# Optimization experiments

Measured on AMD Instinct MI355X. Metric: run time of the kernel, lower is better.

The kernel has to match this reference:

```python
import jax, jax.numpy as jnp
import numpy as np

H, E, K = 1024, 8, 2  # hidden_size, num_experts, top_k
B, S = 2, 4096


def setup_inputs() -> dict:
    key = jax.random.key(0)
    ks = jax.random.split(key, 5)
    s = 1.0 / np.sqrt(H)
    return {
        "x": jax.random.normal(ks[0], (B, S, H), dtype=jnp.float32),
        "ln_scale": jnp.ones((H,), jnp.float32),
        "ln_bias": jnp.zeros((H,), jnp.float32),
        "w1": (jax.random.normal(ks[1], (H, H), jnp.float32) * s),
        "b1": jnp.zeros((H,), jnp.float32),
        "w2": (jax.random.normal(ks[2], (H, E), jnp.float32) * s),
        "b2": jnp.zeros((E,), jnp.float32),
        "We": (jax.random.normal(ks[3], (E, H, H), jnp.float32) * s),
        "be": jnp.zeros((E, H), jnp.float32),
    }


def _layernorm(x, scale, bias, eps=1e-5):
    m = jnp.mean(x, axis=-1, keepdims=True)
    v = jnp.var(x, axis=-1, keepdims=True)
    return (x - m) * jax.lax.rsqrt(v + eps) * scale + bias


def reference(x, ln_scale, ln_bias, w1, b1, w2, b2, We, be):
    b, s, h = x.shape
    # --- router (BaseRouter): LN -> MLP -> softmax -> top-k -> renorm ---
    xn = _layernorm(x, ln_scale, ln_bias)
    hmid = jax.nn.relu(xn @ w1 + b1)
    logits = hmid @ w2 + b2                      # [B,S,E]
    probs = jax.nn.softmax(logits, axis=-1)
    topk_p, topk_i = jax.lax.top_k(probs, K)     # [B,S,K]
    topk_p = topk_p / jnp.sum(topk_p, axis=-1, keepdims=True)
    # sparse combine weights [B,S,E]: renormalized top-k gate, 0 elsewhere
    cw = jnp.sum(topk_p[..., None] * jax.nn.one_hot(topk_i, E, dtype=x.dtype), axis=-2)
    # --- expert dispatch / weighted combine ---
    t = b * s
    xf = x.reshape(t, h)
    cwf = cw.reshape(t, E)
    ye = jnp.einsum('th,ehd->etd', xf, We) + be[:, None, :]   # [E,T,H]
    out = jnp.einsum('te,etd->td', cwf, ye).reshape(b, s, h)
    # --- aux load-balance loss ---
    mean_p = jnp.mean(probs, axis=(0, 1))        # [E]
    aux = jnp.sum(mean_p * jnp.log(mean_p * E + 1e-9))
    return out, aux
```

## Files before the change

### kernel.cpp

```cpp
#include <hip/hip_runtime.h>
#include <hip/hip_fp16.h>

#define H 1024
#define E 8
#define TT 8192

typedef __attribute__((ext_vector_type(8))) short bf16x8;
typedef __attribute__((ext_vector_type(4))) float f32x4;

__device__ __forceinline__ unsigned short f2bf(float f) {
  unsigned int u = __float_as_uint(f);
  u += 0x7fffu + ((u >> 16) & 1u);
  return (unsigned short)(u >> 16);
}

__device__ __forceinline__ int swz(int row, int c) {
  return (row << 5) | (((c ^ (row >> 1)) & 3) << 3);
}

__device__ __forceinline__ void gld16(void* lds, const void* g) {
  __builtin_amdgcn_global_load_lds((const __attribute__((address_space(1))) void*)g,
                                   (__attribute__((address_space(3))) void*)lds, 16, 0, 0);
}

__global__ __launch_bounds__(64) void k_init(int* cnt, double* psum) {
  int t = threadIdx.x;
  if (t < E) { cnt[t] = 0; psum[t] = 0.0; }
}

__global__ __launch_bounds__(256) void k_cast_we(const float* __restrict__ we, unsigned short* __restrict__ wet) {
  __shared__ unsigned short tile[32][33];
  int e = blockIdx.z;
  int kb = blockIdx.x << 5, nb = blockIdx.y << 5;
  int t = threadIdx.x;
  int cc = t & 31, rr = t >> 5;
  size_t base = (size_t)e * H * H;
#pragma unroll
  for (int r = 0; r < 4; ++r) {
    int k = kb + rr + (r << 3);
    tile[rr + (r << 3)][cc] = f2bf(we[base + (size_t)k * H + nb + cc]);
  }
  __syncthreads();
#pragma unroll
  for (int r = 0; r < 4; ++r) {
    int n = nb + rr + (r << 3);
    wet[base + (size_t)n * H + kb + cc] = tile[cc][rr + (r << 3)];
  }
}

__global__ __launch_bounds__(256) void k_cast_w1(const float* __restrict__ w1, const float* __restrict__ lsc,
                                                 unsigned short* __restrict__ w1h, unsigned short* __restrict__ w1l) {
  __shared__ float tile[32][33];
  int kb = blockIdx.x << 5, nb = blockIdx.y << 5;
  int t = threadIdx.x;
  int cc = t & 31, rr = t >> 5;
#pragma unroll
  for (int r = 0; r < 4; ++r) {
    int k = kb + rr + (r << 3);
    tile[rr + (r << 3)][cc] = w1[(size_t)k * H + nb + cc] * lsc[k];
  }
  __syncthreads();
#pragma unroll
  for (int r = 0; r < 4; ++r) {
    int n = nb + rr + (r << 3);
    float v = tile[cc][rr + (r << 3)];
    unsigned short h = f2bf(v);
    float hv = __uint_as_float((unsigned)h << 16);
    unsigned short l = f2bf(v - hv);
    w1h[(size_t)n * H + kb + cc] = h;
    w1l[(size_t)n * H + kb + cc] = l;
  }
}

__global__ __launch_bounds__(256) void k_b1a(const float* __restrict__ w1, const float* __restrict__ lbi,
                                             float* __restrict__ part) {
  int bk = blockIdx.x, t = threadIdx.x;
  float a0 = 0, a1 = 0, a2 = 0, a3 = 0;
  for (int kk = 0; kk < 16; ++kk) {
    int k = (bk << 4) + kk;
    float lb = lbi[k];
    const float* row = &w1[(size_t)k * H];
    a0 = fmaf(lb, row[t], a0);
    a1 = fmaf(lb, row[t + 256], a1);
    a2 = fmaf(lb, row[t + 512], a2);
    a3 = fmaf(lb, row[t + 768], a3);
  }
  part[bk * H + t] = a0;
  part[bk * H + t + 256] = a1;
  part[bk * H + t + 512] = a2;
  part[bk * H + t + 768] = a3;
}

__global__ __launch_bounds__(256) void k_b1b(const float* __restrict__ part, const float* __restrict__ b1,
                                             float* __restrict__ b1eff) {
  int n = (blockIdx.x << 8) + threadIdx.x;
  float s = b1[n];
  for (int j = 0; j < 64; ++j) s += part[j * H + n];
  b1eff[n] = s;
}

__global__ __launch_bounds__(256) void k_stats(const float* __restrict__ x, unsigned short* __restrict__ xb,
                                               unsigned short* __restrict__ zh, unsigned short* __restrict__ zl) {
  int tok = blockIdx.x, t = threadIdx.x;
  const float4 v = *reinterpret_cast<const float4*>(&x[(size_t)tok * H + (t << 2)]);
  float s = v.x + v.y + v.z + v.w;
  float ss = v.x * v.x + v.y * v.y + v.z * v.z + v.w * v.w;
#pragma unroll
  for (int off = 32; off; off >>= 1) { s += __shfl_down(s, off); ss += __shfl_down(ss, off); }
  __shared__ float red[4][2];
  int lane = t & 63, wv = t >> 6;
  if (lane == 0) { red[wv][0] = s; red[wv][1] = ss; }
  __syncthreads();
  float fs = red[0][0] + red[1][0] + red[2][0] + red[3][0];
  float fss = red[0][1] + red[1][1] + red[2][1] + red[3][1];
  float mean = fs * (1.0f / H);
  float var = fss * (1.0f / H) - mean * mean;
  float rstd = rsqrtf(var + 1e-5f);
  float mb = -mean * rstd;
  size_t base = (size_t)tok * H + (t << 2);
  ushort4 ob;
  ob.x = f2bf(v.x); ob.y = f2bf(v.y); ob.z = f2bf(v.z); ob.w = f2bf(v.w);
  *reinterpret_cast<ushort4*>(&xb[base]) = ob;
  float zz[4];
  zz[0] = fmaf(v.x, rstd, mb); zz[1] = fmaf(v.y, rstd, mb);
  zz[2] = fmaf(v.z, rstd, mb); zz[3] = fmaf(v.w, rstd, mb);
  ushort4 oh, ol;
  unsigned u0 = __float_as_uint(zz[0]), u1 = __float_as_uint(zz[1]);
  unsigned u2 = __float_as_uint(zz[2]), u3 = __float_as_uint(zz[3]);
  oh.x = (unsigned short)(u0 >> 16); oh.y = (unsigned short)(u1 >> 16);
  oh.z = (unsigned short)(u2 >> 16); oh.w = (unsigned short)(u3 >> 16);
  float l0 = zz[0] - __uint_as_float(u0 & 0xffff0000u);
  float l1 = zz[1] - __uint_as_float(u1 & 0xffff0000u);
  float l2 = zz[2] - __uint_as_float(u2 & 0xffff0000u);
  float l3 = zz[3] - __uint_as_float(u3 & 0xffff0000u);
  ol.x = (unsigned short)(__float_as_uint(l0) >> 16); ol.y = (unsigned short)(__float_as_uint(l1) >> 16);
  ol.z = (unsigned short)(__float_as_uint(l2) >> 16); ol.w = (unsigned short)(__float_as_uint(l3) >> 16);
  *reinterpret_cast<ushort4*>(&zh[base]) = oh;
  *reinterpret_cast<ushort4*>(&zl[base]) = ol;
}

__global__ __launch_bounds__(256) void k_router_mfma(
    const unsigned short* __restrict__ zh, const unsigned short* __restrict__ zl,
    const unsigned short* __restrict__ w1h,
    const float* __restrict__ b1eff, const float* __restrict__ w2, float* __restrict__ plog) {
  __shared__ __align__(16) short Bt[3][8192];
  int t = threadIdx.x;
  int d = blockIdx.x;
  int l = ((d & 7) << 6) + (d >> 3);
  int bm = (l >> 3) << 7;
  int bnb = l & 7, bn = bnb << 7;
  int w = t >> 6, lane = t & 63;
  int l15 = lane & 15, lgp = lane >> 4;
  int wr = (w >> 1) << 6, wc = (w & 1) << 6;
  int sl = (w << 8) + lane;
  int bo[4];
#pragma unroll
  for (int q = 0; q < 4; ++q) {
    int s = sl + (q << 6);
    int r = s >> 2, cg = (s & 3) ^ ((r >> 1) & 3);
    bo[q] = ((r < 128) ? (bn + r) * H : 1048576 + (bn + r - 128) * H) + (cg << 3);
  }
  int dB = w << 11;
  int zo[4];
#pragma unroll
  for (int i = 0; i < 4; ++i) zo[i] = (bm + wr + (i << 4) + l15) * H + (lgp << 3);
  f32x4 acc[4][4];
#pragma unroll
  for (int i = 0; i < 4; ++i)
#pragma unroll
    for (int j = 0; j < 4; ++j) acc[i][j] = f32x4{0.f, 0.f, 0.f, 0.f};
  bf16x8 ah[3][4], al[3][4];
#pragma unroll
  for (int q = 0; q < 4; ++q) gld16(&Bt[0][dB + (q << 9)], w1h + bo[q]);
#pragma unroll
  for (int q = 0; q < 4; ++q) gld16(&Bt[1][dB + (q << 9)], w1h + bo[q] + 32);
#pragma unroll
  for (int i = 0; i < 4; ++i) {
    ah[0][i] = *(const bf16x8*)(zh + zo[i]);
    al[0][i] = *(const bf16x8*)(zl + zo[i]);
    ah[1][i] = *(const bf16x8*)(zh + zo[i] + 32);
    al[1][i] = *(const bf16x8*)(zl + zo[i] + 32);
  }
#pragma unroll
  for (int kt = 0; kt < 32; ++kt) {
    const int cur = kt % 3;
    if (kt <= 29) {
      const int slot = (kt + 2) % 3, ko = (kt + 2) << 5;
#pragma unroll
      for (int i = 0; i < 4; ++i) {
        ah[slot][i] = *(const bf16x8*)(zh + zo[i] + ko);
        al[slot][i] = *(const bf16x8*)(zl + zo[i] + ko);
      }
    }
    if (kt <= 29) {
      asm volatile("s_waitcnt vmcnt(20)" ::: "memory");
    } else if (kt == 30) {
      asm volatile("s_waitcnt vmcnt(12)" ::: "memory");
    } else {
      asm volatile("s_waitcnt vmcnt(0)" ::: "memory");
    }
    __builtin_amdgcn_sched_barrier(0);
    __builtin_amdgcn_s_barrier();
    __builtin_amdgcn_sched_barrier(0);
    if (kt <= 29) {
      const int bnxt = (kt + 2) % 3, ko = (kt + 2) << 5;
#pragma unroll
      for (int q = 0; q < 4; ++q) gld16(&Bt[bnxt][dB + (q << 9)], w1h + bo[q] + ko);
    }
#pragma unroll
    for (int j = 0; j < 4; ++j) {
      bf16x8 bh = *(const bf16x8*)&Bt[cur][swz(wc + (j << 4) + l15, lgp)];
      bf16x8 bl = *(const bf16x8*)&Bt[cur][swz(128 + wc + (j << 4) + l15, lgp)];
#pragma unroll
      for (int i = 0; i < 4; ++i) {
        acc[i][j] = __builtin_amdgcn_mfma_f32_16x16x32_bf16(ah[cur][i], bh, acc[i][j], 0, 0, 0);
        acc[i][j] = __builtin_amdgcn_mfma_f32_16x16x32_bf16(ah[cur][i], bl, acc[i][j], 0, 0, 0);
        acc[i][j] = __builtin_amdgcn_mfma_f32_16x16x32_bf16(al[cur][i], bh, acc[i][j], 0, 0, 0);
      }
    }
  }
  float w2r[4][8], b1r[4];
#pragma unroll
  for (int j = 0; j < 4; ++j) {
    int col = bn + wc + (j << 4) + l15;
    float4 p0 = *(const float4*)&w2[(size_t)col * E];
    float4 p1 = *(const float4*)&w2[(size_t)col * E + 4];
    w2r[j][0] = p0.x; w2r[j][1] = p0.y; w2r[j][2] = p0.z; w2r[j][3] = p0.w;
    w2r[j][4] = p1.x; w2r[j][5] = p1.y; w2r[j][6] = p1.z; w2r[j][7] = p1.w;
    b1r[j] = b1eff[col];
  }
#pragma unroll
  for (int i = 0; i < 4; ++i)
#pragma unroll
    for (int j = 0; j < 4; ++j)
#pragma unroll
      for (int r = 0; r < 4; ++r) acc[i][j][r] = fmaxf(acc[i][j][r] + b1r[j], 0.f);
  int wh = wc >> 6;
  size_t pbase = ((size_t)(bnb * 2 + wh) * TT + bm) * E;
#pragma unroll
  for (int e = 0; e < E; ++e) {
    float se[4][4];
#pragma unroll
    for (int i = 0; i < 4; ++i)
#pragma unroll
      for (int r = 0; r < 4; ++r)
        se[i][r] = acc[i][0][r] * w2r[0][e] + acc[i][1][r] * w2r[1][e] +
                   acc[i][2][r] * w2r[2][e] + acc[i][3][r] * w2r[3][e];
#pragma unroll
    for (int off = 1; off < 16; off <<= 1)
#pragma unroll
      for (int i = 0; i < 4; ++i)
#pragma unroll
        for (int r = 0; r < 4; ++r) se[i][r] += __shfl_xor(se[i][r], off);
    if (l15 == 0) {
#pragma unroll
      for (int i = 0; i < 4; ++i)
#pragma unroll
        for (int r = 0; r < 4; ++r) {
          int row = wr + (i << 4) + (lgp << 2) + r;
          plog[pbase + (size_t)row * E + e] = se[i][r];
        }
    }
  }
}

__global__ __launch_bounds__(256) void k_top(const float* __restrict__ plog, const float* __restrict__ b2,
                                             int* __restrict__ topE, float* __restrict__ topW,
                                             int* __restrict__ listIdx, float* __restrict__ listW,
                                             int* __restrict__ cnt, double* __restrict__ psum) {
  int t = threadIdx.x, lane = t & 63;
  int tok = (blockIdx.x << 8) + t;
  float lg[E], p[E];
  float4 ba = *reinterpret_cast<const float4*>(b2);
  float4 bb = *reinterpret_cast<const float4*>(b2 + 4);
  lg[0] = ba.x; lg[1] = ba.y; lg[2] = ba.z; lg[3] = ba.w;
  lg[4] = bb.x; lg[5] = bb.y; lg[6] = bb.z; lg[7] = bb.w;
#pragma unroll
  for (int nb = 0; nb < 16; ++nb) {
    const float* pp = &plog[((size_t)nb * TT + tok) * E];
    float4 q0 = *reinterpret_cast<const float4*>(pp);
    float4 q1 = *reinterpret_cast<const float4*>(pp + 4);
    lg[0] += q0.x; lg[1] += q0.y; lg[2] += q0.z; lg[3] += q0.w;
    lg[4] += q1.x; lg[5] += q1.y; lg[6] += q1.z; lg[7] += q1.w;
  }
  float m = lg[0];
#pragma unroll
  for (int e = 1; e < E; ++e) m = fmaxf(m, lg[e]);
  float s = 0.f;
#pragma unroll
  for (int e = 0; e < E; ++e) { p[e] = __expf(lg[e] - m); s += p[e]; }
  float inv = 1.f / s;
#pragma unroll
  for (int e = 0; e < E; ++e) p[e] *= inv;
  {
    float ps[E];
#pragma unroll
    for (int e = 0; e < E; ++e) ps[e] = p[e];
#pragma unroll
    for (int off = 1; off < 64; off <<= 1)
#pragma unroll
      for (int e = 0; e < E; ++e) ps[e] += __shfl_xor(ps[e], off);
    if (lane == 0)
#pragma unroll
      for (int e = 0; e < E; ++e) atomicAdd(&psum[e], (double)ps[e]);
  }
  int e0 = 0;
#pragma unroll
  for (int e = 1; e < E; ++e) if (p[e] > p[e0]) e0 = e;
  int e1 = (e0 == 0) ? 1 : 0;
#pragma unroll
  for (int e = 0; e < E; ++e) if (e != e0 && p[e] > p[e1]) e1 = e;
  float rsw = 1.f / (p[e0] + p[e1]);
  float w0 = p[e0] * rsw, w1v = p[e1] * rsw;
  topE[tok << 1] = e0; topE[(tok << 1) + 1] = e1;
  topW[tok << 1] = w0; topW[(tok << 1) + 1] = w1v;
  unsigned long long lt = (1ull << lane) - 1ull;
#pragma unroll
  for (int e = 0; e < E; ++e) {
    unsigned long long m0 = __ballot(e0 == e);
    unsigned long long m1 = __ballot(e1 == e);
    int n0 = __popcll(m0), total = n0 + __popcll(m1);
    if (total == 0) continue;
    int leader = __ffsll(m0 | m1) - 1;
    int base = 0;
    if (lane == leader) base = atomicAdd(&cnt[e], total);
    base = __shfl(base, leader);
    if (e0 == e) {
      int pos = e * TT + base + __popcll(m0 & lt);
      listIdx[pos] = (tok << 1); listW[pos] = w0;
    }
    if (e1 == e) {
      int pos = e * TT + base + n0 + __popcll(m1 & lt);
      listIdx[pos] = (tok << 1) | 1; listW[pos] = w1v;
    }
  }
}

__global__ __launch_bounds__(256) void k_expert_gemm(const unsigned short* __restrict__ xb,
                                                     const unsigned short* __restrict__ wet,
                                                     const int* __restrict__ listIdx, const float* __restrict__ listW,
                                                     const int* __restrict__ cnt, unsigned short* __restrict__ ys) {
  int d = blockIdx.x;
  int l = ((d & 7) << 8) + (d >> 3);
  int e = l >> 8;
  int lx = l & 255;
  int bx = lx >> 2, by = lx & 3;
  int c = cnt[e];
  int r0 = bx << 7;
  if (r0 >= c) return;
  int n0 = by << 8;
  __shared__ __align__(16) short A[3][4096];
  __shared__ __align__(16) short Bs[3][8192];
  __shared__ int gi[128];
  __shared__ float gw[128];
  int t = threadIdx.x;
  if (t < 128) {
    int rr = r0 + t;
    gi[t] = (rr < c) ? listIdx[e * TT + rr] : -1;
    gw[t] = (rr < c) ? listW[e * TT + rr] : 0.f;
  }
  __syncthreads();
  int w = t >> 6, lane = t & 63;
  int l15 = lane & 15, lgp = lane >> 4;
  int wr = (w >> 1) << 6;
  int wc = (w & 1) << 7;
  int rA0 = t >> 2, cA0 = (t & 3) ^ ((rA0 >> 1) & 3);
  int sA1 = t + 256;
  int rA1 = sA1 >> 2, cA1 = (sA1 & 3) ^ ((rA1 >> 1) & 3);
  int pk0 = gi[rA0], pk1 = gi[rA1];
  const unsigned short* srcA0 = xb + (size_t)((pk0 < 0) ? 0 : (pk0 >> 1)) * H + (cA0 << 3);
  const unsigned short* srcA1 = xb + (size_t)((pk1 < 0) ? 0 : (pk1 >> 1)) * H + (cA1 << 3);
  int ebase = e << 20;
  int boB[4];
#pragma unroll
  for (int q = 0; q < 4; ++q) {
    int s = t + (q << 8);
    int r = s >> 2, cg = (s & 3) ^ ((r >> 1) & 3);
    boB[q] = ebase + (n0 + r) * H + (cg << 3);
  }
  int dA = w << 9;
  int dB = w << 9;
  f32x4 acc[4][8];
#pragma unroll
  for (int i = 0; i < 4; ++i)
#pragma unroll
    for (int j = 0; j < 8; ++j) acc[i][j] = f32x4{0.f, 0.f, 0.f, 0.f};
#pragma unroll
  for (int pt = 0; pt < 3; ++pt) {
    const int ko = pt << 5;
    gld16(&A[pt][dA], srcA0 + ko);
    gld16(&A[pt][dA + 2048], srcA1 + ko);
#pragma unroll
    for (int q = 0; q < 4; ++q) gld16(&Bs[pt][dB + (q << 11)], wet + boB[q] + ko);
  }
#pragma unroll
  for (int kt = 0; kt < 32; ++kt) {
    if (kt <= 29) {
      asm volatile("s_waitcnt vmcnt(12)" ::: "memory");
    } else if (kt == 30) {
      asm volatile("s_waitcnt vmcnt(6)" ::: "memory");
    } else {
      asm volatile("s_waitcnt vmcnt(0)" ::: "memory");
    }
    __builtin_amdgcn_sched_barrier(0);
    __builtin_amdgcn_s_barrier();
    __builtin_amdgcn_sched_barrier(0);
    const int bb = kt % 3;
    bf16x8 aq[4];
#pragma unroll
    for (int i = 0; i < 4; ++i) aq[i] = *(const bf16x8*)&A[bb][swz(wr + (i << 4) + l15, lgp)];
#pragma unroll
    for (int j = 0; j < 8; ++j) {
      bf16x8 bq = *(const bf16x8*)&Bs[bb][swz(wc + (j << 4) + l15, lgp)];
#pragma unroll
      for (int i = 0; i < 4; ++i)
        acc[i][j] = __builtin_amdgcn_mfma_f32_16x16x32_bf16(aq[i], bq, acc[i][j], 0, 0, 0);
    }
    if (kt <= 28) {
      __builtin_amdgcn_sched_barrier(0);
      __builtin_amdgcn_s_barrier();
      const int ko = (kt + 3) << 5;
      gld16(&A[bb][dA], srcA0 + ko);
      gld16(&A[bb][dA + 2048], srcA1 + ko);
#pragma unroll
      for (int q = 0; q < 4; ++q) gld16(&Bs[bb][dB + (q << 11)], wet + boB[q] + ko);
    }
  }
#pragma unroll
  for (int i = 0; i < 4; ++i) {
#pragma unroll
    for (int r = 0; r < 4; ++r) {
      int row = wr + (i << 4) + (lgp << 2) + r;
      int pk = gi[row];
      if (pk < 0) continue;
      int tok = pk >> 1, slot = pk & 1;
      float wgt = gw[row];
      size_t ob = ((size_t)slot * TT + tok) * H + n0 + wc + l15;
#pragma unroll
      for (int j = 0; j < 8; ++j) ys[ob + (j << 4)] = __half_as_ushort(__float2half(wgt * acc[i][j][r]));
    }
  }
}

__global__ __launch_bounds__(256) void k_combine(const unsigned short* __restrict__ ys, const int* __restrict__ topE,
                                                 const float* __restrict__ topW, const float* __restrict__ be,
                                                 float* __restrict__ out) {
  int tok = blockIdx.x, t = threadIdx.x;
  int e0 = topE[tok << 1], e1 = topE[(tok << 1) + 1];
  float w0 = topW[tok << 1], w1v = topW[(tok << 1) + 1];
  int h = t << 2;
  size_t base = (size_t)tok * H + h;
  ushort4 a = *reinterpret_cast<const ushort4*>(&ys[base]);
  ushort4 b = *reinterpret_cast<const ushort4*>(&ys[(size_t)TT * H + base]);
  float4 b0 = *reinterpret_cast<const float4*>(&be[e0 * H + h]);
  float4 b1v = *reinterpret_cast<const float4*>(&be[e1 * H + h]);
  float4 o;
  o.x = __half2float(__ushort_as_half(a.x)) + __half2float(__ushort_as_half(b.x)) + w0 * b0.x + w1v * b1v.x;
  o.y = __half2float(__ushort_as_half(a.y)) + __half2float(__ushort_as_half(b.y)) + w0 * b0.y + w1v * b1v.y;
  o.z = __half2float(__ushort_as_half(a.z)) + __half2float(__ushort_as_half(b.z)) + w0 * b0.z + w1v * b1v.z;
  o.w = __half2float(__ushort_as_half(a.w)) + __half2float(__ushort_as_half(b.w)) + w0 * b0.w + w1v * b1v.w;
  *reinterpret_cast<float4*>(&out[base]) = o;
}

__global__ __launch_bounds__(64) void k_aux(const double* __restrict__ psum, float* __restrict__ outAux) {
  if (threadIdx.x == 0) {
    double a = 0.0;
    for (int e = 0; e < E; ++e) {
      double mp = psum[e] / (double)TT;
      a += mp * log(mp * (double)E + 1e-9);
    }
    outAux[0] = (float)a;
  }
}

extern "C" void kernel_launch(void* const* d_in, const int* in_sizes, int n_in, void* d_out, int out_size, void* d_ws,
                              size_t ws_size, hipStream_t stream) {
  const float* x = (const float*)d_in[0];
  const float* lsc = (const float*)d_in[1];
  const float* lbi = (const float*)d_in[2];
  const float* w1 = (const float*)d_in[3];
  const float* b1 = (const float*)d_in[4];
  const float* w2 = (const float*)d_in[5];
  const float* b2 = (const float*)d_in[6];
  const float* we = (const float*)d_in[7];
  const float* be = (const float*)d_in[8];
  float* out = (float*)d_out;
  char* ws = (char*)d_ws;

  char* p = ws;
  int* topE = (int*)p; p += TT * 2 * 4;
  float* topW = (float*)p; p += TT * 2 * 4;
  int* listIdx = (int*)p; p += E * TT * 4;
  float* listW = (float*)p; p += E * TT * 4;
  int* cnt = (int*)p; p += 256;
  double* psum = (double*)p; p += 2048;
  float* b1eff = (float*)p; p += H * 4;
  float* part = (float*)p; p += 64 * H * 4;
  unsigned short* xb = (unsigned short*)(ws + (2ull << 20));
  unsigned short* zh = (unsigned short*)(ws + (18ull << 20));
  unsigned short* zl = (unsigned short*)(ws + (34ull << 20));
  unsigned short* w1h = (unsigned short*)(ws + (50ull << 20));
  unsigned short* w1l = (unsigned short*)(ws + (52ull << 20));
  float* plog = (float*)(ws + (54ull << 20));
  unsigned short* wet = (unsigned short*)(ws + (18ull << 20));
  unsigned short* ys = (unsigned short*)(ws + (34ull << 20));

  k_init<<<1, 64, 0, stream>>>(cnt, psum);
  k_cast_w1<<<dim3(32, 32), 256, 0, stream>>>(w1, lsc, w1h, w1l);
  k_b1a<<<64, 256, 0, stream>>>(w1, lbi, part);
  k_b1b<<<4, 256, 0, stream>>>(part, b1, b1eff);
  k_stats<<<TT, 256, 0, stream>>>(x, xb, zh, zl);
  k_router_mfma<<<512, 256, 0, stream>>>(zh, zl, w1h, b1eff, w2, plog);
  k_top<<<TT / 256, 256, 0, stream>>>(plog, b2, topE, topW, listIdx, listW, cnt, psum);
  k_cast_we<<<dim3(32, 32, E), 256, 0, stream>>>(we, wet);
  k_expert_gemm<<<2048, 256, 0, stream>>>(xb, wet, listIdx, listW, cnt, ys);
  k_combine<<<TT, 256, 0, stream>>>(ys, topE, topW, be, out);
  k_aux<<<1, 64, 0, stream>>>(psum, out + (size_t)TT * H);
}
```

Before: 252.1 us.

## Compact expert GEMM work list and shrink tiles to 128x128 with double buffering

Adds a single-block scheduler kernel that builds a dense, expert-interleaved list of (expert, row-block, column-block) work items from the per-expert token counts, so the grouped GEMM launches only useful blocks instead of early-exiting empty ones. The expert GEMM tile is reduced from 128x256 to 128x128, and the triple-buffered LDS pipeline becomes a double buffer with prefetch before the wait, plus s_setprio around the MFMA block. The intent is better load balance and occupancy across CUs with less LDS per block. The cost is an extra tiny kernel launch, more blocks each loading the A tile twice as often, and a shallower prefetch depth that can expose more memory latency.

```diff
diff --git a/kernel.cpp b/kernel.cpp
--- a/kernel.cpp
+++ b/kernel.cpp
@@ -336,21 +336,38 @@
   }
 }
 
+#define WL_SLOTS 2560
+__global__ __launch_bounds__(256) void k_sched(const int* __restrict__ cnt, int* __restrict__ workList) {
+  int t = threadIdx.x;
+  for (int i = t; i < WL_SLOTS; i += 256) workList[i] = -1;
+  __syncthreads();
+  if (t < E) {
+    int e = t;
+    int nb = (cnt[e] + 127) >> 7;
+    int ov = 2048 + (e << 6);
+    int g = 0;
+    for (int bx = 0; bx < nb; ++bx) {
+      for (int by = 0; by < 8; ++by) {
+        int item = (e << 12) | (bx << 4) | by;
+        int slot = (g < 256) ? ((g << 3) + e) : ov++;
+        workList[slot] = item;
+        ++g;
+      }
+    }
+  }
+}
+
 __global__ __launch_bounds__(256) void k_expert_gemm(const unsigned short* __restrict__ xb,
                                                      const unsigned short* __restrict__ wet,
                                                      const int* __restrict__ listIdx, const float* __restrict__ listW,
-                                                     const int* __restrict__ cnt, unsigned short* __restrict__ ys) {
-  int d = blockIdx.x;
-  int l = ((d & 7) << 8) + (d >> 3);
-  int e = l >> 8;
-  int lx = l & 255;
-  int bx = lx >> 2, by = lx & 3;
+                                                     const int* __restrict__ cnt, const int* __restrict__ workList,
+                                                     unsigned short* __restrict__ ys) {
+  int item = workList[blockIdx.x];
+  if (item < 0) return;
+  int e = item >> 12, bx = (item >> 4) & 255, by = item & 15;
   int c = cnt[e];
-  int r0 = bx << 7;
-  if (r0 >= c) return;
-  int n0 = by << 8;
-  __shared__ __align__(16) short A[3][4096];
-  __shared__ __align__(16) short Bs[3][8192];
+  int r0 = bx << 7, n0 = by << 7;
+  __shared__ __align__(16) short A[2][4096], Bs[2][4096];
   __shared__ int gi[128];
   __shared__ float gw[128];
   int t = threadIdx.x;
@@ -362,68 +379,54 @@
   __syncthreads();
   int w = t >> 6, lane = t & 63;
   int l15 = lane & 15, lgp = lane >> 4;
-  int wr = (w >> 1) << 6;
-  int wc = (w & 1) << 7;
-  int rA0 = t >> 2, cA0 = (t & 3) ^ ((rA0 >> 1) & 3);
-  int sA1 = t + 256;
-  int rA1 = sA1 >> 2, cA1 = (sA1 & 3) ^ ((rA1 >> 1) & 3);
+  int wr = (w >> 1) << 6, wc = (w & 1) << 6;
+  int s0 = (w << 7) + lane, s1 = s0 + 64;
+  int rA0 = s0 >> 2, cg0 = (s0 & 3) ^ ((rA0 >> 1) & 3);
+  int rA1 = s1 >> 2, cg1 = (s1 & 3) ^ ((rA1 >> 1) & 3);
   int pk0 = gi[rA0], pk1 = gi[rA1];
-  const unsigned short* srcA0 = xb + (size_t)((pk0 < 0) ? 0 : (pk0 >> 1)) * H + (cA0 << 3);
-  const unsigned short* srcA1 = xb + (size_t)((pk1 < 0) ? 0 : (pk1 >> 1)) * H + (cA1 << 3);
-  int ebase = e << 20;
-  int boB[4];
-#pragma unroll
-  for (int q = 0; q < 4; ++q) {
-    int s = t + (q << 8);
-    int r = s >> 2, cg = (s & 3) ^ ((r >> 1) & 3);
-    boB[q] = ebase + (n0 + r) * H + (cg << 3);
-  }
-  int dA = w << 9;
-  int dB = w << 9;
-  f32x4 acc[4][8];
+  const unsigned short* srcA0 = xb + (size_t)((pk0 < 0) ? 0 : (pk0 >> 1)) * H + (cg0 << 3);
+  const unsigned short* srcA1 = xb + (size_t)((pk1 < 0) ? 0 : (pk1 >> 1)) * H + (cg1 << 3);
+  size_t wbase = (size_t)e * H * H;
+  const unsigned short* srcB0 = wet + wbase + (size_t)(n0 + rA0) * H + (cg0 << 3);
+  const unsigned short* srcB1 = wet + wbase + (size_t)(n0 + rA1) * H + (cg1 << 3);
+  int d0 = (w << 10), d1 = d0 + 512;
+  f32x4 acc[4][4];
 #pragma unroll
   for (int i = 0; i < 4; ++i)
 #pragma unroll
-    for (int j = 0; j < 8; ++j) acc[i][j] = f32x4{0.f, 0.f, 0.f, 0.f};
-#pragma unroll
-  for (int pt = 0; pt < 3; ++pt) {
-    const int ko = pt << 5;
-    gld16(&A[pt][dA], srcA0 + ko);
-    gld16(&A[pt][dA + 2048], srcA1 + ko);
-#pragma unroll
-    for (int q = 0; q < 4; ++q) gld16(&Bs[pt][dB + (q << 11)], wet + boB[q] + ko);
-  }
+    for (int j = 0; j < 4; ++j) acc[i][j] = f32x4{0.f, 0.f, 0.f, 0.f};
+  gld16(&A[0][d0], srcA0); gld16(&A[0][d1], srcA1);
+  gld16(&Bs[0][d0], srcB0); gld16(&Bs[0][d1], srcB1);
 #pragma unroll
   for (int kt = 0; kt < 32; ++kt) {
-    if (kt <= 29) {
-      asm volatile("s_waitcnt vmcnt(12)" ::: "memory");
-    } else if (kt == 30) {
-      asm volatile("s_waitcnt vmcnt(6)" ::: "memory");
+    const int cur = kt & 1, nxt = cur ^ 1;
+    if (kt < 31) {
+      const int ko = (kt + 1) << 5;
+      gld16(&A[nxt][d0], srcA0 + ko); gld16(&A[nxt][d1], srcA1 + ko);
+      gld16(&Bs[nxt][d0], srcB0 + ko); gld16(&Bs[nxt][d1], srcB1 + ko);
+      asm volatile("s_waitcnt vmcnt(4)" ::: "memory");
     } else {
       asm volatile("s_waitcnt vmcnt(0)" ::: "memory");
     }
     __builtin_amdgcn_sched_barrier(0);
     __builtin_amdgcn_s_barrier();
     __builtin_amdgcn_sched_barrier(0);
-    const int bb = kt % 3;
+    bf16x8 bq[4];
+#pragma unroll
+    for (int j = 0; j < 4; ++j) bq[j] = *(const bf16x8*)&Bs[cur][swz(wc + (j << 4) + l15, lgp)];
     bf16x8 aq[4];
 #pragma unroll
-    for (int i = 0; i < 4; ++i) aq[i] = *(const bf16x8*)&A[bb][swz(wr + (i << 4) + l15, lgp)];
-#pragma unroll
-    for (int j = 0; j < 8; ++j) {
-      bf16x8 bq = *(const bf16x8*)&Bs[bb][swz(wc + (j << 4) + l15, lgp)];
-#pragma unroll
-      for (int i = 0; i < 4; ++i)
-        acc[i][j] = __builtin_amdgcn_mfma_f32_16x16x32_bf16(aq[i], bq, acc[i][j], 0, 0, 0);
-    }
-    if (kt <= 28) {
+    for (int i = 0; i < 4; ++i) aq[i] = *(const bf16x8*)&A[cur][swz(wr + (i << 4) + l15, lgp)];
+    __builtin_amdgcn_s_setprio(1);
+#pragma unroll
+    for (int i = 0; i < 4; ++i)
+#pragma unroll
+      for (int j = 0; j < 4; ++j)
+        acc[i][j] = __builtin_amdgcn_mfma_f32_16x16x32_bf16(aq[i], bq[j], acc[i][j], 0, 0, 0);
+    __builtin_amdgcn_s_setprio(0);
+    if (kt < 31) {
       __builtin_amdgcn_sched_barrier(0);
       __builtin_amdgcn_s_barrier();
-      const int ko = (kt + 3) << 5;
-      gld16(&A[bb][dA], srcA0 + ko);
-      gld16(&A[bb][dA + 2048], srcA1 + ko);
-#pragma unroll
-      for (int q = 0; q < 4; ++q) gld16(&Bs[bb][dB + (q << 11)], wet + boB[q] + ko);
     }
   }
 #pragma unroll
@@ -437,7 +440,7 @@
       float wgt = gw[row];
       size_t ob = ((size_t)slot * TT + tok) * H + n0 + wc + l15;
 #pragma unroll
-      for (int j = 0; j < 8; ++j) ys[ob + (j << 4)] = __half_as_ushort(__float2half(wgt * acc[i][j][r]));
+      for (int j = 0; j < 4; ++j) ys[ob + (j << 4)] = __half_as_ushort(__float2half(wgt * acc[i][j][r]));
     }
   }
 }
@@ -496,6 +499,7 @@
   double* psum = (double*)p; p += 2048;
   float* b1eff = (float*)p; p += H * 4;
   float* part = (float*)p; p += 64 * H * 4;
+  int* workList = (int*)p; p += WL_SLOTS * 4;
   unsigned short* xb = (unsigned short*)(ws + (2ull << 20));
   unsigned short* zh = (unsigned short*)(ws + (18ull << 20));
   unsigned short* zl = (unsigned short*)(ws + (34ull << 20));
@@ -512,8 +516,9 @@
   k_stats<<<TT, 256, 0, stream>>>(x, xb, zh, zl);
   k_router_mfma<<<512, 256, 0, stream>>>(zh, zl, w1h, b1eff, w2, plog);
   k_top<<<TT / 256, 256, 0, stream>>>(plog, b2, topE, topW, listIdx, listW, cnt, psum);
+  k_sched<<<1, 256, 0, stream>>>(cnt, workList);
   k_cast_we<<<dim3(32, 32, E), 256, 0, stream>>>(we, wet);
-  k_expert_gemm<<<2048, 256, 0, stream>>>(xb, wet, listIdx, listW, cnt, ys);
+  k_expert_gemm<<<WL_SLOTS, 256, 0, stream>>>(xb, wet, listIdx, listW, cnt, workList, ys);
   k_combine<<<TT, 256, 0, stream>>>(ys, topE, topW, be, out);
   k_aux<<<1, 64, 0, stream>>>(psum, out + (size_t)TT * H);
 }
```

New measurement: 245.3 us. -2.7%, faster.
